# Performance work log

Hardware: AMD Instinct MI355X
Metric: run time of the kernel (lower is better)

Reference implementation:

```python
import jax, jax.numpy as jnp
import numpy as np

H = 512      # hidden_size
E = 256      # encoding_size
L = 64       # latent_dim
O = 2        # output_size
NH = 4       # num_heads
HD = H // NH # head dim
BS = 1024
S = 100      # encoded source length
T = 30       # decode steps


def setup_inputs() -> dict:
    key = jax.random.key(0)
    ks = jax.random.split(key, 26)
    def p(k, shape, s=0.05):
        return jax.random.normal(k, shape, dtype=jnp.float32) * s
    return {
        "encoded": jax.random.normal(ks[0], (BS, S, E), dtype=jnp.float32),
        "z": jax.random.normal(ks[1], (BS, T, L), dtype=jnp.float32),
        # MultiheadAttention params (separate q/k/v projections since kdim!=embed_dim)
        "q_w": p(ks[2], (H, H)), "k_w": p(ks[3], (H, E)), "v_w": p(ks[4], (H, E)),
        "q_b": p(ks[5], (H,)), "k_b": p(ks[6], (H,)), "v_b": p(ks[7], (H,)),
        "out_w": p(ks[8], (H, H)), "out_b": p(ks[9], (H,)),
        # fc_layer1: Linear(H+L, H)
        "fc1_w": p(ks[10], (H, H + L)), "fc1_b": p(ks[11], (H,)),
        # LSTMCell 1 and 2 (gate order i,f,g,o)
        "l1_wih": p(ks[12], (4 * H, H)), "l1_whh": p(ks[13], (4 * H, H)),
        "l1_bih": p(ks[14], (4 * H,)), "l1_bhh": p(ks[15], (4 * H,)),
        "l2_wih": p(ks[16], (4 * H, H)), "l2_whh": p(ks[17], (4 * H, H)),
        "l2_bih": p(ks[18], (4 * H,)), "l2_bhh": p(ks[19], (4 * H,)),
        # fc_layer2: H -> H/2 -> H/4 -> O
        "fc2a_w": p(ks[20], (H // 2, H)), "fc2a_b": p(ks[21], (H // 2,)),
        "fc2b_w": p(ks[22], (H // 4, H // 2)), "fc2b_b": p(ks[23], (H // 4,)),
        "fc2c_w": p(ks[24], (O, H // 4)), "fc2c_b": p(ks[25], (O,)),
    }


def _lrelu(x):
    return jnp.where(x >= 0, x, 0.2 * x)


def _lstm_cell(x, h, c, wih, whh, bih, bhh):
    g = x @ wih.T + bih + h @ whh.T + bhh
    i, f, gg, o = jnp.split(g, 4, axis=-1)
    c2 = jax.nn.sigmoid(f) * c + jax.nn.sigmoid(i) * jnp.tanh(gg)
    h2 = jax.nn.sigmoid(o) * jnp.tanh(c2)
    return h2, c2


def _forward(encoded, z, q_w, k_w, v_w, q_b, k_b, v_b, out_w, out_b,
             fc1_w, fc1_b, l1_wih, l1_whh, l1_bih, l1_bhh,
             l2_wih, l2_whh, l2_bih, l2_bhh,
             fc2a_w, fc2a_b, fc2b_w, fc2b_b, fc2c_w, fc2c_b):
    bs, s, _ = encoded.shape
    # K/V projections depend only on encoded -> compute once: [bs, NH, S, HD]
    k = (encoded @ k_w.T + k_b).reshape(bs, s, NH, HD).transpose(0, 2, 1, 3)
    v = (encoded @ v_w.T + v_b).reshape(bs, s, NH, HD).transpose(0, 2, 1, 3)
    scale = 1.0 / jnp.sqrt(jnp.float32(HD))

    def step(carry, zt):
        att_in, h1, c1, h2, c2 = carry  # all [bs, H]
        # single-query attention (query len 1); dropout inactive in eval
        q = ((att_in @ q_w.T + q_b) * scale).reshape(bs, NH, HD)
        attw = jax.nn.softmax(jnp.einsum('bnd,bnsd->bns', q, k), axis=-1)
        att = jnp.einsum('bns,bnsd->bnd', attw, v).reshape(bs, H)
        att = att @ out_w.T + out_b
        out = _lrelu(jnp.concatenate([att, zt], axis=-1) @ fc1_w.T + fc1_b)
        h1, c1 = _lstm_cell(out, h1, c1, l1_wih, l1_whh, l1_bih, l1_bhh)
        h2, c2 = _lstm_cell(h1, h2, c2, l2_wih, l2_whh, l2_bih, l2_bhh)
        y = _lrelu(h2 @ fc2a_w.T + fc2a_b)
        y = _lrelu(y @ fc2b_w.T + fc2b_b)
        y = jnp.tanh(y @ fc2c_w.T + fc2c_b)  # [bs, O]
        return (h2, h1, c1, h2, c2), y

    zer = jnp.zeros((bs, H), dtype=encoded.dtype)
    init = (zer, zer, zer, zer, zer)
    _, ys = jax.lax.scan(step, init, jnp.swapaxes(z, 0, 1))  # ys: [T, bs, O]
    return jnp.swapaxes(ys, 0, 1)  # [bs, T, O]


def reference(encoded, z, q_w, k_w, v_w, q_b, k_b, v_b, out_w, out_b,
              fc1_w, fc1_b, l1_wih, l1_whh, l1_bih, l1_bhh,
              l2_wih, l2_whh, l2_bih, l2_bhh,
              fc2a_w, fc2a_b, fc2b_w, fc2b_b, fc2c_w, fc2c_b):
    return _forward(encoded, z, q_w, k_w, v_w, q_b, k_b, v_b, out_w, out_b,
                    fc1_w, fc1_b, l1_wih, l1_whh, l1_bih, l1_bhh,
                    l2_wih, l2_whh, l2_bih, l2_bhh,
                    fc2a_w, fc2a_b, fc2b_w, fc2b_b, fc2c_w, fc2c_b)
```

## Files before the change

### kernel.cpp

```cpp
#include <hip/hip_runtime.h>


#define DEVI __device__ __forceinline__

typedef _Float16 f16x8 __attribute__((ext_vector_type(8)));
typedef _Float16 f16x4 __attribute__((ext_vector_type(4)));
typedef float    f32x4 __attribute__((ext_vector_type(4)));
typedef unsigned u32x4 __attribute__((ext_vector_type(4)));
typedef unsigned u32x2 __attribute__((ext_vector_type(2)));

#define BSZ 1024
#define SEQ 100
#define ENC 256
#define HID 512
#define LAT 64
#define TT  30

DEVI float lrelu(float v) { return v >= 0.f ? v : 0.2f * v; }
DEVI float sigm(float x)  { return 1.f / (1.f + __expf(-x)); }
DEVI float tanh_f(float x){ return 1.f - 2.f / (1.f + __expf(2.f * x)); }
DEVI unsigned umin2(unsigned a, unsigned b) { return a < b ? a : b; }

DEVI void wait_vm0() { asm volatile("s_waitcnt vmcnt(0)" ::: "memory"); }
DEVI u32x4 ld_sc_b128(const void* p) {
    u32x4 d;
    asm volatile("global_load_dwordx4 %0, %1, off sc0 sc1" : "=v"(d) : "v"(p) : "memory");
    return d;
}
DEVI void st_sc_b128(void* p, u32x4 v) {
    asm volatile("global_store_dwordx4 %0, %1, off sc0 sc1" :: "v"(p), "v"(v) : "memory");
}
DEVI void st_sc_b64(void* p, u32x2 v) {
    asm volatile("global_store_dwordx2 %0, %1, off sc0 sc1" :: "v"(p), "v"(v) : "memory");
}
DEVI void st_sc_b32(void* p, unsigned v) {
    asm volatile("global_store_dword %0, %1, off sc0 sc1" :: "v"(p), "v"(v) : "memory");
}

__global__ __launch_bounds__(256) void zero_ws(uint4* __restrict__ p) {
    uint4 z; z.x = z.y = z.z = z.w = 0u;
    p[(size_t)blockIdx.x * 256 + threadIdx.x] = z;
}

__global__ __launch_bounds__(256) void conv_enc(const float4* __restrict__ src,
                                                f16x4* __restrict__ dst) {
    size_t i = (size_t)blockIdx.x * 256 + threadIdx.x;
    float4 v = src[i];
    f16x4 h;
    h.x = (_Float16)v.x; h.y = (_Float16)v.y; h.z = (_Float16)v.z; h.w = (_Float16)v.w;
    dst[i] = h;
}

__global__ __launch_bounds__(256) void prep_qk(const float* __restrict__ k_w,
                                               const float* __restrict__ q_w,
                                               const float* __restrict__ q_b,
                                               _Float16* __restrict__ C_h,
                                               float* __restrict__ d_f,
                                               _Float16* __restrict__ d_h) {
    const int ne = blockIdx.x, n = ne >> 8, e = ne & 255, tid = threadIdx.x;
    const float scale = 0.08838834764831845f;
    float a0 = 0.f, a1 = 0.f;
    for (int dd = 0; dd < 128; ++dd) {
        float kv = k_w[(n * 128 + dd) * 256 + e];
        a0 += kv * q_w[(n * 128 + dd) * 512 + tid];
        a1 += kv * q_w[(n * 128 + dd) * 512 + 256 + tid];
    }
    C_h[(size_t)ne * 512 + tid]       = (_Float16)(scale * a0);
    C_h[(size_t)ne * 512 + 256 + tid] = (_Float16)(scale * a1);
    float pq = (tid < 128) ? k_w[(n * 128 + tid) * 256 + e] * q_b[n * 128 + tid] : 0.f;
    #pragma unroll
    for (int off = 32; off; off >>= 1) pq += __shfl_down(pq, off);
    __shared__ float red[4];
    if ((tid & 63) == 0) red[tid >> 6] = pq;
    __syncthreads();
    if (tid == 0) {
        float s = scale * (red[0] + red[1] + red[2] + red[3]);
        d_f[ne] = s; d_h[ne] = (_Float16)s;
    }
}

__global__ __launch_bounds__(256) void prep_A(const float* __restrict__ fc1_w,
                                              const float* __restrict__ out_w,
                                              float* __restrict__ A) {
    const int h = blockIdx.x, tid = threadIdx.x;
    float a0 = 0.f, a1 = 0.f;
    for (int m = 0; m < 512; ++m) {
        float fv = fc1_w[h * 576 + m];
        a0 += fv * out_w[m * 512 + tid];
        a1 += fv * out_w[m * 512 + 256 + tid];
    }
    A[(size_t)h * 512 + tid]       = a0;
    A[(size_t)h * 512 + 256 + tid] = a1;
}

__global__ __launch_bounds__(256) void prep_wfc1(const float* __restrict__ A,
                                                 const float* __restrict__ v_w,
                                                 const float* __restrict__ v_b,
                                                 const float* __restrict__ fc1_w,
                                                 const float* __restrict__ out_b,
                                                 const float* __restrict__ fc1_b,
                                                 _Float16* __restrict__ Wfc1,
                                                 float* __restrict__ biasf) {
    const int h = blockIdx.x, tid = threadIdx.x;
    #pragma unroll
    for (int g = 0; g < 4; ++g) {
        float acc = 0.f;
        for (int dd = 0; dd < 128; ++dd)
            acc += A[h * 512 + g * 128 + dd] * v_w[(g * 128 + dd) * 256 + tid];
        Wfc1[(size_t)h * 1088 + g * 256 + tid] = (_Float16)acc;
    }
    if (tid < 64)
        Wfc1[(size_t)h * 1088 + 1024 + tid] = (_Float16)fc1_w[h * 576 + 512 + tid];
    float ps = A[h * 512 + tid] * v_b[tid] + A[h * 512 + 256 + tid] * v_b[256 + tid]
             + fc1_w[h * 576 + tid] * out_b[tid] + fc1_w[h * 576 + 256 + tid] * out_b[256 + tid];
    #pragma unroll
    for (int off = 32; off; off >>= 1) ps += __shfl_down(ps, off);
    __shared__ float red[4];
    if ((tid & 63) == 0) red[tid >> 6] = ps;
    __syncthreads();
    if (tid == 0) biasf[h] = red[0] + red[1] + red[2] + red[3] + fc1_b[h];
}

__global__ __launch_bounds__(256) void prep_lstm(const float* __restrict__ wih,
                                                 const float* __restrict__ whh,
                                                 const float* __restrict__ bih,
                                                 const float* __restrict__ bhh,
                                                 _Float16* __restrict__ Wc,
                                                 float* __restrict__ bc) {
    int idx = blockIdx.x * 256 + threadIdx.x;
    int rp = idx >> 10, cc = idx & 1023;
    int h = rp >> 2, g = rp & 3;
    int rsrc = g * 512 + h;
    float v = (cc < 512) ? wih[(size_t)rsrc * 512 + cc] : whh[(size_t)rsrc * 512 + cc - 512];
    Wc[idx] = (_Float16)v;
    if (idx < 2048) {
        int h2 = idx >> 2, g2 = idx & 3;
        bc[idx] = bih[g2 * 512 + h2] + bhh[g2 * 512 + h2];
    }
}

__global__ __launch_bounds__(256) void prep_fc2c(const float* __restrict__ aw,
                                                 const float* __restrict__ bw,
                                                 const float* __restrict__ cw,
                                                 _Float16* __restrict__ a16,
                                                 _Float16* __restrict__ b16,
                                                 _Float16* __restrict__ c16) {
    int i = blockIdx.x * 256 + threadIdx.x;
    if (i < 131072) a16[i] = (_Float16)aw[i];
    else if (i < 163840) b16[i - 131072] = (_Float16)bw[i - 131072];
    else if (i < 164096) c16[i - 163840] = (_Float16)cw[i - 163840];
}

template <int NTHR, int BM, int BN, int BK, int WM, int WN, bool BYPX>
DEVI void gemm_core_db(char* smem_raw, const _Float16* __restrict__ X, int ldx,
                       const _Float16* __restrict__ W, int ldw, int K,
                       int bm0, int bn0, f32x4* acc) {
    constexpr int LDT = BK + 8;
    _Float16* Xs = (_Float16*)smem_raw;
    _Float16* Ws = Xs + BM * LDT;
    const int tid = threadIdx.x, wave = tid >> 6, lane = tid & 63;
    constexpr int WROWS = BM / WM;
    static_assert(WROWS * (BN / WN) == NTHR / 64, "wave grid mismatch");
    const int wm = wave % WROWS, wn = wave / WROWS;
    constexpr int MT = WM / 16, NT = WN / 16;
    const int q = lane >> 4, m15 = lane & 15;
    constexpr int CPR = BK / 8;
    constexpr int XCH = BM * CPR, WCH = BN * CPR;
    constexpr int XPT = (XCH + NTHR - 1) / NTHR;
    constexpr int WPT = (WCH + NTHR - 1) / NTHR;
    u32x4 xr[XPT], wr[WPT];
    auto ldregs = [&](int k0) {
        #pragma unroll
        for (int c = 0; c < XPT; ++c) {
            int cc = tid + c * NTHR;
            if ((XCH % NTHR) == 0 || cc < XCH) {
                int row = cc / CPR, col = (cc % CPR) * 8;
                const void* px = &X[(size_t)(bm0 + row) * ldx + k0 + col];
                if (BYPX) xr[c] = ld_sc_b128(px);
                else      xr[c] = *(const u32x4*)px;
            }
        }
        #pragma unroll
        for (int c = 0; c < WPT; ++c) {
            int cc = tid + c * NTHR;
            if ((WCH % NTHR) == 0 || cc < WCH) {
                int row = cc / CPR, col = (cc % CPR) * 8;
                wr[c] = *(const u32x4*)&W[(size_t)(bn0 + row) * ldw + k0 + col];
            }
        }
    };
    ldregs(0);
    for (int k0 = 0; k0 < K; k0 += BK) {
        if (BYPX) wait_vm0();
        #pragma unroll
        for (int c = 0; c < XPT; ++c) {
            int cc = tid + c * NTHR;
            if ((XCH % NTHR) == 0 || cc < XCH) {
                int row = cc / CPR, col = (cc % CPR) * 8;
                *(u32x4*)&Xs[row * LDT + col] = xr[c];
            }
        }
        #pragma unroll
        for (int c = 0; c < WPT; ++c) {
            int cc = tid + c * NTHR;
            if ((WCH % NTHR) == 0 || cc < WCH) {
                int row = cc / CPR, col = (cc % CPR) * 8;
                *(u32x4*)&Ws[row * LDT + col] = wr[c];
            }
        }
        __syncthreads();
        if (k0 + BK < K) ldregs(k0 + BK);
        #pragma unroll
        for (int kk = 0; kk < BK / 32; ++kk) {
            f16x8 af[MT], bf[NT];
            #pragma unroll
            for (int i = 0; i < MT; ++i)
                af[i] = *(const f16x8*)&Xs[(wm * WM + i * 16 + m15) * LDT + kk * 32 + q * 8];
            #pragma unroll
            for (int j = 0; j < NT; ++j)
                bf[j] = *(const f16x8*)&Ws[(wn * WN + j * 16 + m15) * LDT + kk * 32 + q * 8];
            #pragma unroll
            for (int i = 0; i < MT; ++i)
                #pragma unroll
                for (int j = 0; j < NT; ++j)
                    acc[i * NT + j] = __builtin_amdgcn_mfma_f32_16x16x32_f16(af[i], bf[j], acc[i * NT + j], 0, 0, 0);
        }
        __syncthreads();
    }
}

template <int NTHR, int BM, int BN, int WM, int WN, int ACT>
DEVI void epi_staged(char* smem_raw, const f32x4* acc, const float* __restrict__ bias,
                     _Float16* __restrict__ out, int ldo, int bm0, int bn0) {
    constexpr int LDS_ = BN + 4;
    float* accs = (float*)smem_raw;
    const int tid = threadIdx.x, wave = tid >> 6, lane = tid & 63;
    constexpr int WROWS = BM / WM;
    const int wm = wave % WROWS, wn = wave / WROWS;
    constexpr int MT = WM / 16, NT = WN / 16;
    const int q = lane >> 4, m15 = lane & 15;
    #pragma unroll
    for (int i = 0; i < MT; ++i) {
        #pragma unroll
        for (int j = 0; j < NT; ++j) {
            int cl = wn * WN + j * 16 + m15;
            float bv = bias[bn0 + cl];
            #pragma unroll
            for (int r = 0; r < 4; ++r) {
                int rl = wm * WM + i * 16 + q * 4 + r;
                float v = acc[i * NT + j][r] + bv;
                if (ACT == 1) v = lrelu(v);
                accs[rl * LDS_ + cl] = v;
            }
        }
    }
    __syncthreads();
    constexpr int CH = BN / 8, ITEMS = BM * CH;
    #pragma unroll
    for (int base = 0; base < ITEMS; base += NTHR) {
        int idx = base + tid;
        if ((ITEMS % NTHR) == 0 || idx < ITEMS) {
            int row = idx / CH, ch = idx % CH;
            const float* src = &accs[row * LDS_ + ch * 8];
            f16x8 o;
            #pragma unroll
            for (int k = 0; k < 8; ++k) o[k] = (_Float16)src[k];
            st_sc_b128(&out[(size_t)(bm0 + row) * ldo + bn0 + ch * 8],
                       __builtin_bit_cast(u32x4, o));
        }
    }
    __syncthreads();
}

DEVI void gbar(unsigned* bars, int grp, int sub, unsigned want) {
    wait_vm0();
    __syncthreads();
    if (threadIdx.x == 0) {
        st_sc_b32(&bars[grp * 16 + sub], want);
        unsigned spins = 0;
        for (;;) {
            u32x4 a = ld_sc_b128(&bars[grp * 16 + 0]);
            u32x4 b = ld_sc_b128(&bars[grp * 16 + 4]);
            u32x4 c = ld_sc_b128(&bars[grp * 16 + 8]);
            u32x4 d = ld_sc_b128(&bars[grp * 16 + 12]);
            wait_vm0();
            unsigned mn = umin2(umin2(umin2(a[0], a[1]), umin2(a[2], a[3])),
                          umin2(umin2(umin2(b[0], b[1]), umin2(b[2], b[3])),
                          umin2(umin2(umin2(c[0], c[1]), umin2(c[2], c[3])),
                                umin2(umin2(d[0], d[1]), umin2(d[2], d[3])))));
            if (mn >= want) break;
            __builtin_amdgcn_s_sleep(1);
            if (++spins > (1u << 17)) break;
        }
        asm volatile("" ::: "memory");
    }
    __syncthreads();
}

DEVI void attn_one(const _Float16* encs, const _Float16* gs, float* sc, float* wsm,
                   f32x4* part, const float* __restrict__ z,
                   _Float16* __restrict__ eb, int gi, int b, int t) {
    const int tid = threadIdx.x;
    {
        const int grpq = tid >> 4, l16 = tid & 15, n = grpq & 3, soff = grpq >> 2;
        const f16x8 g0 = *(const f16x8*)&gs[gi * 1024 + n * 256 + l16 * 8];
        const f16x8 g1 = *(const f16x8*)&gs[gi * 1024 + n * 256 + 128 + l16 * 8];
        for (int it = 0; it < 13; ++it) {
            int s = it * 8 + soff;
            if (s < SEQ) {
                const f16x8 e0 = *(const f16x8*)&encs[s * ENC + l16 * 8];
                const f16x8 e1 = *(const f16x8*)&encs[s * ENC + 128 + l16 * 8];
                float p = 0.f;
                #pragma unroll
                for (int j = 0; j < 8; ++j)
                    p += (float)e0[j] * (float)g0[j] + (float)e1[j] * (float)g1[j];
                p += __shfl_xor(p, 1); p += __shfl_xor(p, 2);
                p += __shfl_xor(p, 4); p += __shfl_xor(p, 8);
                if (l16 == 0) sc[n * 128 + s] = p;
            }
        }
    }
    __syncthreads();
    const int wv = tid >> 6, ln = tid & 63;
    if (wv < 4) {
        float v0 = sc[wv * 128 + ln];
        float v1 = (ln < SEQ - 64) ? sc[wv * 128 + 64 + ln] : -1e30f;
        float m = fmaxf(v0, v1);
        #pragma unroll
        for (int off = 32; off; off >>= 1) m = fmaxf(m, __shfl_xor(m, off));
        float e0 = __expf(v0 - m);
        float e1 = (ln < SEQ - 64) ? __expf(v1 - m) : 0.f;
        float ss = e0 + e1;
        #pragma unroll
        for (int off = 32; off; off >>= 1) ss += __shfl_xor(ss, off);
        float inv = 1.f / ss;
        wsm[wv * 128 + ln] = e0 * inv;
        if (ln < SEQ - 64) wsm[wv * 128 + 64 + ln] = e1 * inv;
    }
    __syncthreads();
    {
        const int n = wv & 3, half = wv >> 2;
        float a0 = 0.f, a1 = 0.f, a2 = 0.f, a3 = 0.f;
        const int sBeg = half * 50, sEnd = sBeg + 50;
        #pragma unroll 5
        for (int s = sBeg; s < sEnd; ++s) {
            f16x4 e4 = *(const f16x4*)&encs[s * ENC + ln * 4];
            float w = wsm[n * 128 + s];
            a0 += w * (float)e4.x; a1 += w * (float)e4.y;
            a2 += w * (float)e4.z; a3 += w * (float)e4.w;
        }
        f32x4 pv; pv[0] = a0; pv[1] = a1; pv[2] = a2; pv[3] = a3;
        part[wv * 64 + ln] = pv;
    }
    __syncthreads();
    if (tid < 128) {
        int n = tid >> 5, t8 = tid & 31;
        f32x4 a  = part[n * 64 + t8 * 2];
        f32x4 b2 = part[n * 64 + t8 * 2 + 1];
        f32x4 c  = part[(n + 4) * 64 + t8 * 2];
        f32x4 d  = part[(n + 4) * 64 + t8 * 2 + 1];
        f16x8 o;
        o[0] = (_Float16)(a[0] + c[0]); o[1] = (_Float16)(a[1] + c[1]);
        o[2] = (_Float16)(a[2] + c[2]); o[3] = (_Float16)(a[3] + c[3]);
        o[4] = (_Float16)(b2[0] + d[0]); o[5] = (_Float16)(b2[1] + d[1]);
        o[6] = (_Float16)(b2[2] + d[2]); o[7] = (_Float16)(b2[3] + d[3]);
        st_sc_b128(&eb[(size_t)b * 1088 + n * 256 + t8 * 8],
                   __builtin_bit_cast(u32x4, o));
    } else if (tid < 144) {
        int k = tid - 128;
        float4 zv = *(const float4*)&z[((size_t)b * TT + t) * 64 + k * 4];
        f16x4 zh;
        zh.x = (_Float16)zv.x; zh.y = (_Float16)zv.y;
        zh.z = (_Float16)zv.z; zh.w = (_Float16)zv.w;
        st_sc_b64(&eb[(size_t)b * 1088 + 1024 + k * 4],
                  __builtin_bit_cast(u32x2, zh));
    }
    __syncthreads();
}

DEVI void attn_phase(char* smem_all, u32x4 (&er)[3][7],
                     const _Float16* __restrict__ G, const float* __restrict__ z,
                     _Float16* __restrict__ eb, int b0, int t) {
    _Float16* encP  = (_Float16*)smem_all;
    char* scratch   = smem_all + 51200;
    _Float16* stage = (_Float16*)scratch;
    _Float16* gs    = (_Float16*)(scratch + 51200);
    float* sc       = (float*)(scratch + 59392);
    float* wsm      = (float*)(scratch + 61440);
    f32x4* part     = (f32x4*)(scratch + 63488);
    const int tid = threadIdx.x;
    {
        int row = tid >> 7, idx = tid & 127;
        u32x4 gv = ld_sc_b128(&G[(size_t)(b0 + row) * 1024 + idx * 8]);
        wait_vm0();
        *(u32x4*)&gs[row * 1024 + idx * 8] = gv;
    }
    __syncthreads();
    attn_one(encP, gs, sc, wsm, part, z, eb, 0, b0, t);
    #pragma unroll
    for (int i = 0; i < 3; ++i) {
        {
            u32x4* dst = (u32x4*)stage;
            #pragma unroll
            for (int k = 0; k < 6; ++k) dst[tid + k * 512] = er[i][k];
            if (tid < 128) dst[tid + 3072] = er[i][6];
        }
        __syncthreads();
        attn_one(stage, gs, sc, wsm, part, z, eb, i + 1, b0 + 1 + i, t);
    }
}

DEVI void lstm_phase(char* smem, const _Float16* __restrict__ X,
                     const _Float16* __restrict__ W, const float* __restrict__ bias,
                     float (&cr)[8], _Float16* __restrict__ hA, int ldA,
                     _Float16* __restrict__ hB, int ldB, int bm0, int bn0) {
    f32x4 acc[4] = {};
    gemm_core_db<512, 64, 128, 128, 32, 32, true>(smem, X, 1024, W, 1024, 1024, bm0, bn0, acc);
    float* accs = (float*)smem;
    const int tid = threadIdx.x, wave = tid >> 6, lane = tid & 63;
    const int wm = wave & 1, wn = wave >> 1, q = lane >> 4, m15 = lane & 15;
    #pragma unroll
    for (int i = 0; i < 2; ++i) {
        #pragma unroll
        for (int j = 0; j < 2; ++j) {
            int cl = wn * 32 + j * 16 + m15;
            float bv = bias[bn0 + cl];
            #pragma unroll
            for (int r = 0; r < 4; ++r) {
                int rl = wm * 32 + i * 16 + q * 4 + r;
                accs[rl * 132 + cl] = acc[i * 2 + j][r] + bv;
            }
        }
    }
    __syncthreads();
    if (tid < 256) {
        int bl = tid >> 2, ch = tid & 3;
        const float4* gp = (const float4*)&accs[bl * 132 + ch * 32];
        f16x8 hv;
        #pragma unroll
        for (int j = 0; j < 8; ++j) {
            float4 g4 = gp[j];
            float cn = sigm(g4.y) * cr[j] + sigm(g4.x) * tanh_f(g4.z);
            cr[j] = cn;
            hv[j] = (_Float16)(sigm(g4.w) * tanh_f(cn));
        }
        int h0 = (bn0 >> 2) + ch * 8, gb = bm0 + bl;
        u32x4 hb = __builtin_bit_cast(u32x4, hv);
        st_sc_b128(&hA[(size_t)gb * ldA + h0], hb);
        st_sc_b128(&hB[(size_t)gb * ldB + h0], hb);
    }
    __syncthreads();
}

DEVI void fc2_512(char* smem, const _Float16* __restrict__ h2n,
                  const _Float16* __restrict__ Wa, const float* __restrict__ ab,
                  const _Float16* __restrict__ Wb, const float* __restrict__ bb,
                  const _Float16* __restrict__ Wc, const float* __restrict__ cb,
                  float* __restrict__ out, int b0, int t) {
    _Float16* h2s = (_Float16*)smem;
    _Float16* y1s = h2s + 16 * 520;
    _Float16* y2s = y1s + 16 * 264;
    const int tid = threadIdx.x, wave = tid >> 6, lane = tid & 63;
    const int q = lane >> 4, m15 = lane & 15;
    u32x4 hv[2];
    #pragma unroll
    for (int c = 0; c < 2; ++c) {
        int cc = tid + c * 512, row = cc >> 6, col = (cc & 63) * 8;
        hv[c] = ld_sc_b128(&h2n[(size_t)(b0 + row) * 512 + col]);
    }
    wait_vm0();
    #pragma unroll
    for (int c = 0; c < 2; ++c) {
        int cc = tid + c * 512, row = cc >> 6, col = (cc & 63) * 8;
        *(u32x4*)&h2s[row * 520 + col] = hv[c];
    }
    __syncthreads();
    {
        f32x4 acc[2] = {};
        #pragma unroll 4
        for (int kk = 0; kk < 16; ++kk) {
            f16x8 af = *(const f16x8*)&h2s[m15 * 520 + kk * 32 + q * 8];
            #pragma unroll
            for (int j = 0; j < 2; ++j) {
                int n = wave * 32 + j * 16 + m15;
                f16x8 bf = *(const f16x8*)&Wa[(size_t)n * 512 + kk * 32 + q * 8];
                acc[j] = __builtin_amdgcn_mfma_f32_16x16x32_f16(af, bf, acc[j], 0, 0, 0);
            }
        }
        #pragma unroll
        for (int j = 0; j < 2; ++j) {
            int col = wave * 32 + j * 16 + m15;
            float bv = ab[col];
            #pragma unroll
            for (int r = 0; r < 4; ++r)
                y1s[(q * 4 + r) * 264 + col] = (_Float16)lrelu(acc[j][r] + bv);
        }
    }
    __syncthreads();
    {
        f32x4 acc[1] = {};
        #pragma unroll
        for (int kk = 0; kk < 8; ++kk) {
            f16x8 af = *(const f16x8*)&y1s[m15 * 264 + kk * 32 + q * 8];
            int n = wave * 16 + m15;
            f16x8 bf = *(const f16x8*)&Wb[(size_t)n * 256 + kk * 32 + q * 8];
            acc[0] = __builtin_amdgcn_mfma_f32_16x16x32_f16(af, bf, acc[0], 0, 0, 0);
        }
        int col = wave * 16 + m15;
        float bv = bb[col];
        #pragma unroll
        for (int r = 0; r < 4; ++r)
            y2s[(q * 4 + r) * 136 + col] = (_Float16)lrelu(acc[0][r] + bv);
    }
    __syncthreads();
    if (tid < 32) {
        int r = tid >> 1, o = tid & 1;
        float acc = cb[o];
        #pragma unroll 8
        for (int k = 0; k < 128; ++k)
            acc += (float)Wc[o * 128 + k] * (float)y2s[r * 136 + k];
        out[((size_t)(b0 + r) * TT + t) * 2 + o] = tanhf(acc);
    }
}

struct DecP {
    const _Float16* encH;
    const float* z;
    _Float16* eb;
    const _Float16* Wfc1;  const float* biasf;
    const _Float16* L1W;   const float* L1b;
    const _Float16* L2W;   const float* L2b;
    const _Float16* C_h;   const float* d_f;  const _Float16* d_h;
    const _Float16* fa;    const float* fab;
    const _Float16* fb;    const float* fbb;
    const _Float16* fcw;   const float* fcb;
    _Float16* xh1[2];  _Float16* xh2[2];  _Float16* h2n;  _Float16* G;
    float* out;
    unsigned* bars;
};

__global__ __launch_bounds__(512, 1) void decoder(DecP p) {
    __shared__ __align__(16) char smem[122880];
    char* scratch = smem + 51200;
    const int blk = blockIdx.x, tid = threadIdx.x;
    const int grp = blk >> 4, sub = blk & 15;
    const int b0a = blk * 4;
    const int bm0 = grp * 64;
    float c1r[8] = {}, c2r[8] = {};
    u32x4 er[3][7];
    unsigned want = 0;
    {
        const u32x4* s0 = (const u32x4*)(p.encH + (size_t)b0a * (SEQ * ENC));
        u32x4* encP = (u32x4*)smem;
        #pragma unroll
        for (int k = 0; k < 6; ++k) encP[tid + k * 512] = s0[tid + k * 512];
        if (tid < 128) encP[tid + 3072] = s0[tid + 3072];
        #pragma unroll
        for (int i = 0; i < 3; ++i) {
            const u32x4* si = (const u32x4*)(p.encH + (size_t)(b0a + 1 + i) * (SEQ * ENC));
            #pragma unroll
            for (int k = 0; k < 6; ++k) er[i][k] = si[tid + k * 512];
            if (tid < 128) er[i][6] = si[tid + 3072];
        }
    }
    if (tid < 128) {
        u32x4 v = *(const u32x4*)&p.d_h[tid * 8];
        #pragma unroll
        for (int i = 0; i < 4; ++i)
            st_sc_b128(&p.G[(size_t)(b0a + i) * 1024 + tid * 8], v);
    }
    wait_vm0();
    __syncthreads();
    for (int t = 0; t < TT; ++t) {
        const int pt = t & 1;
        attn_phase(smem, er, p.G, p.z, p.eb, b0a, t);
        gbar(p.bars, grp, sub, ++want);
        {
            f32x4 acc[1] = {};
            gemm_core_db<512, 64, 32, 64, 16, 16, true>(scratch, p.eb, 1088, p.Wfc1, 1088, 1088,
                                                        bm0, sub * 32, acc);
            epi_staged<512, 64, 32, 16, 16, 1>(scratch, acc, p.biasf, p.xh1[pt], 1024, bm0, sub * 32);
        }
        gbar(p.bars, grp, sub, ++want);
        lstm_phase(scratch, p.xh1[pt], p.L1W, p.L1b, c1r,
                   p.xh2[pt], 1024, p.xh1[pt ^ 1] + 512, 1024, bm0, sub * 128);
        gbar(p.bars, grp, sub, ++want);
        lstm_phase(scratch, p.xh2[pt], p.L2W, p.L2b, c2r,
                   p.h2n, 512, p.xh2[pt ^ 1] + 512, 1024, bm0, sub * 128);
        gbar(p.bars, grp, sub, ++want);
        if (t < TT - 1) {
            f32x4 acc[2] = {};
            gemm_core_db<512, 64, 64, 128, 16, 32, true>(scratch, p.h2n, 512, p.C_h, 512, 512,
                                                         bm0, sub * 64, acc);
            epi_staged<512, 64, 64, 16, 32, 0>(scratch, acc, p.d_f, p.G, 1024, bm0, sub * 64);
        }
        if (sub < 4)
            fc2_512(scratch, p.h2n, p.fa, p.fab, p.fb, p.fbb, p.fcw, p.fcb,
                    p.out, bm0 + sub * 16, t);
        if (t < TT - 1) gbar(p.bars, grp, sub, ++want);
    }
}

extern "C" void kernel_launch(void* const* d_in, const int* in_sizes, int n_in,
                              void* d_out, int out_size, void* d_ws, size_t ws_size,
                              hipStream_t stream) {
    const float* encoded = (const float*)d_in[0];
    const float* z       = (const float*)d_in[1];
    const float* q_w     = (const float*)d_in[2];
    const float* k_w     = (const float*)d_in[3];
    const float* v_w     = (const float*)d_in[4];
    const float* q_b     = (const float*)d_in[5];
    const float* v_b     = (const float*)d_in[7];
    const float* out_w   = (const float*)d_in[8];
    const float* out_b   = (const float*)d_in[9];
    const float* fc1_w   = (const float*)d_in[10];
    const float* fc1_b   = (const float*)d_in[11];
    const float* l1_wih  = (const float*)d_in[12];
    const float* l1_whh  = (const float*)d_in[13];
    const float* l1_bih  = (const float*)d_in[14];
    const float* l1_bhh  = (const float*)d_in[15];
    const float* l2_wih  = (const float*)d_in[16];
    const float* l2_whh  = (const float*)d_in[17];
    const float* l2_bih  = (const float*)d_in[18];
    const float* l2_bhh  = (const float*)d_in[19];
    const float* fc2a_w  = (const float*)d_in[20];
    const float* fc2a_b  = (const float*)d_in[21];
    const float* fc2b_w  = (const float*)d_in[22];
    const float* fc2b_b  = (const float*)d_in[23];
    const float* fc2c_w  = (const float*)d_in[24];
    const float* fc2c_b  = (const float*)d_in[25];
    float* out = (float*)d_out;

    char* p = (char*)d_ws;
    auto take = [&](size_t bytes) { char* r = p; p += (bytes + 255) & ~(size_t)255; return r; };
    _Float16* encH  = (_Float16*)take(52428800);
    _Float16* C_h   = (_Float16*)take(1048576);
    _Float16* Wfc1  = (_Float16*)take(1114112);
    _Float16* L1W   = (_Float16*)take(4194304);
    _Float16* L2W   = (_Float16*)take(4194304);
    _Float16* fc2a16= (_Float16*)take(262144);
    _Float16* fc2b16= (_Float16*)take(65536);
    _Float16* fc2c16= (_Float16*)take(512);
    _Float16* eb    = (_Float16*)take(2228224);
    _Float16* h2n   = (_Float16*)take(1048576);
    char* zreg = p;
    _Float16* xh1a = (_Float16*)take(2097152);
    _Float16* xh1b = (_Float16*)take(2097152);
    _Float16* xh2a = (_Float16*)take(2097152);
    _Float16* xh2b = (_Float16*)take(2097152);
    unsigned* bars = (unsigned*)take(4096);
    _Float16* G   = (_Float16*)take(2097152);
    float* A      = (float*)take(1048576);
    float* d_f    = (float*)take(4096);
    _Float16* d_h = (_Float16*)take(2048);
    float* biasf  = (float*)take(2048);
    float* L1b    = (float*)take(8192);
    float* L2b    = (float*)take(8192);
    (void)in_sizes; (void)n_in; (void)out_size; (void)ws_size;

    zero_ws<<<2049, 256, 0, stream>>>((uint4*)zreg);
    conv_enc<<<25600, 256, 0, stream>>>((const float4*)encoded, (f16x4*)encH);
    prep_qk<<<1024, 256, 0, stream>>>(k_w, q_w, q_b, C_h, d_f, d_h);
    prep_A<<<512, 256, 0, stream>>>(fc1_w, out_w, A);
    prep_wfc1<<<512, 256, 0, stream>>>(A, v_w, v_b, fc1_w, out_b, fc1_b, Wfc1, biasf);
    prep_lstm<<<8192, 256, 0, stream>>>(l1_wih, l1_whh, l1_bih, l1_bhh, L1W, L1b);
    prep_lstm<<<8192, 256, 0, stream>>>(l2_wih, l2_whh, l2_bih, l2_bhh, L2W, L2b);
    prep_fc2c<<<641, 256, 0, stream>>>(fc2a_w, fc2b_w, fc2c_w, fc2a16, fc2b16, fc2c16);

    DecP dp;
    dp.encH = encH; dp.z = z; dp.eb = eb;
    dp.Wfc1 = Wfc1; dp.biasf = biasf;
    dp.L1W = L1W; dp.L1b = L1b; dp.L2W = L2W; dp.L2b = L2b;
    dp.C_h = C_h; dp.d_f = d_f; dp.d_h = d_h;
    dp.fa = fc2a16; dp.fab = fc2a_b; dp.fb = fc2b16; dp.fbb = fc2b_b;
    dp.fcw = fc2c16; dp.fcb = fc2c_b;
    dp.xh1[0] = xh1a; dp.xh1[1] = xh1b;
    dp.xh2[0] = xh2a; dp.xh2[1] = xh2b;
    dp.h2n = h2n; dp.G = G;
    dp.out = out; dp.bars = bars;
    void* params[] = { &dp };
    if (hipLaunchCooperativeKernel((const void*)decoder, dim3(256), dim3(512),
                                   params, 0, stream) != hipSuccess) {
        decoder<<<256, 512, 0, stream>>>(dp);
    }
}
```

Before: 3.133 ms.

## Keep two encoder rows in LDS and stream the rest from global per step

Instead of holding three encoder rows in registers (er[3][7]) and one in LDS, the kernel now keeps two encoder batch rows resident in an enlarged LDS buffer. It reloads the other two from global memory each step, prefetching each into registers while the previous attention body runs. The attention weighted-sum now uses only four waves over the full sequence, with no partial-sum reduction pass and its extra barrier. This frees a large block of registers and trims the synchronisation, at the cost of re-reading two encoder rows per step from L2/HBM and using more LDS.

```diff
diff --git a/kernel.cpp b/kernel.cpp
--- a/kernel.cpp
+++ b/kernel.cpp
@@ -297,14 +297,14 @@
     __syncthreads();
 }
 
-DEVI void attn_one(const _Float16* encs, const _Float16* gs, float* sc, float* wsm,
-                   f32x4* part, const float* __restrict__ z,
-                   _Float16* __restrict__ eb, int gi, int b, int t) {
+DEVI void attn_body(const _Float16* encs, const _Float16* gs, float* sc, float* wsm,
+                    const float* __restrict__ z, _Float16* __restrict__ eb,
+                    int b, int t) {
     const int tid = threadIdx.x;
     {
         const int grpq = tid >> 4, l16 = tid & 15, n = grpq & 3, soff = grpq >> 2;
-        const f16x8 g0 = *(const f16x8*)&gs[gi * 1024 + n * 256 + l16 * 8];
-        const f16x8 g1 = *(const f16x8*)&gs[gi * 1024 + n * 256 + 128 + l16 * 8];
+        const f16x8 g0 = *(const f16x8*)&gs[n * 256 + l16 * 8];
+        const f16x8 g1 = *(const f16x8*)&gs[n * 256 + 128 + l16 * 8];
         for (int it = 0; it < 13; ++it) {
             int s = it * 8 + soff;
             if (s < SEQ) {
@@ -338,76 +338,72 @@
         if (ln < SEQ - 64) wsm[wv * 128 + 64 + ln] = e1 * inv;
     }
     __syncthreads();
-    {
-        const int n = wv & 3, half = wv >> 2;
+    if (wv < 4) {
         float a0 = 0.f, a1 = 0.f, a2 = 0.f, a3 = 0.f;
-        const int sBeg = half * 50, sEnd = sBeg + 50;
         #pragma unroll 5
-        for (int s = sBeg; s < sEnd; ++s) {
+        for (int s = 0; s < SEQ; ++s) {
             f16x4 e4 = *(const f16x4*)&encs[s * ENC + ln * 4];
-            float w = wsm[n * 128 + s];
+            float w = wsm[wv * 128 + s];
             a0 += w * (float)e4.x; a1 += w * (float)e4.y;
             a2 += w * (float)e4.z; a3 += w * (float)e4.w;
         }
-        f32x4 pv; pv[0] = a0; pv[1] = a1; pv[2] = a2; pv[3] = a3;
-        part[wv * 64 + ln] = pv;
-    }
-    __syncthreads();
-    if (tid < 128) {
-        int n = tid >> 5, t8 = tid & 31;
-        f32x4 a  = part[n * 64 + t8 * 2];
-        f32x4 b2 = part[n * 64 + t8 * 2 + 1];
-        f32x4 c  = part[(n + 4) * 64 + t8 * 2];
-        f32x4 d  = part[(n + 4) * 64 + t8 * 2 + 1];
-        f16x8 o;
-        o[0] = (_Float16)(a[0] + c[0]); o[1] = (_Float16)(a[1] + c[1]);
-        o[2] = (_Float16)(a[2] + c[2]); o[3] = (_Float16)(a[3] + c[3]);
-        o[4] = (_Float16)(b2[0] + d[0]); o[5] = (_Float16)(b2[1] + d[1]);
-        o[6] = (_Float16)(b2[2] + d[2]); o[7] = (_Float16)(b2[3] + d[3]);
-        st_sc_b128(&eb[(size_t)b * 1088 + n * 256 + t8 * 8],
-                   __builtin_bit_cast(u32x4, o));
-    } else if (tid < 144) {
-        int k = tid - 128;
-        float4 zv = *(const float4*)&z[((size_t)b * TT + t) * 64 + k * 4];
+        f16x4 o;
+        o.x = (_Float16)a0; o.y = (_Float16)a1; o.z = (_Float16)a2; o.w = (_Float16)a3;
+        st_sc_b64(&eb[(size_t)b * 1088 + wv * 256 + ln * 4],
+                  __builtin_bit_cast(u32x2, o));
+    } else if (wv == 4 && ln < 16) {
+        float4 zv = *(const float4*)&z[((size_t)b * TT + t) * 64 + ln * 4];
         f16x4 zh;
         zh.x = (_Float16)zv.x; zh.y = (_Float16)zv.y;
         zh.z = (_Float16)zv.z; zh.w = (_Float16)zv.w;
-        st_sc_b64(&eb[(size_t)b * 1088 + 1024 + k * 4],
+        st_sc_b64(&eb[(size_t)b * 1088 + 1024 + ln * 4],
                   __builtin_bit_cast(u32x2, zh));
     }
     __syncthreads();
 }
 
-DEVI void attn_phase(char* smem_all, u32x4 (&er)[3][7],
-                     const _Float16* __restrict__ G, const float* __restrict__ z,
+DEVI void attn_phase(char* smem, const _Float16* __restrict__ G,
+                     const _Float16* __restrict__ encH, const float* __restrict__ z,
                      _Float16* __restrict__ eb, int b0, int t) {
-    _Float16* encP  = (_Float16*)smem_all;
-    char* scratch   = smem_all + 51200;
-    _Float16* stage = (_Float16*)scratch;
-    _Float16* gs    = (_Float16*)(scratch + 51200);
-    float* sc       = (float*)(scratch + 59392);
-    float* wsm      = (float*)(scratch + 61440);
-    f32x4* part     = (f32x4*)(scratch + 63488);
+    _Float16* encP0 = (_Float16*)smem;
+    _Float16* encP1 = (_Float16*)(smem + 51200);
+    float* sc       = (float*)(smem + 102400);
+    float* wsm      = (float*)(smem + 104448);
+    _Float16* gs    = (_Float16*)(smem + 106496);
+    _Float16* stage = (_Float16*)(smem + 108544);
     const int tid = threadIdx.x;
-    {
-        int row = tid >> 7, idx = tid & 127;
-        u32x4 gv = ld_sc_b128(&G[(size_t)(b0 + row) * 1024 + idx * 8]);
-        wait_vm0();
-        *(u32x4*)&gs[row * 1024 + idx * 8] = gv;
-    }
-    __syncthreads();
-    attn_one(encP, gs, sc, wsm, part, z, eb, 0, b0, t);
-    #pragma unroll
-    for (int i = 0; i < 3; ++i) {
-        {
-            u32x4* dst = (u32x4*)stage;
-            #pragma unroll
-            for (int k = 0; k < 6; ++k) dst[tid + k * 512] = er[i][k];
-            if (tid < 128) dst[tid + 3072] = er[i][6];
-        }
-        __syncthreads();
-        attn_one(stage, gs, sc, wsm, part, z, eb, i + 1, b0 + 1 + i, t);
-    }
+    const int grow = tid >> 7, gidx = tid & 127;
+    u32x4 gv = ld_sc_b128(&G[(size_t)(b0 + grow) * 1024 + gidx * 8]);
+    u32x4 r[7];
+    auto ldenc = [&](int b) {
+        const u32x4* src = (const u32x4*)(encH + (size_t)b * (SEQ * ENC));
+        #pragma unroll
+        for (int i = 0; i < 6; ++i) r[i] = src[tid + i * 512];
+        if (tid < 128) r[6] = src[tid + 3072];
+    };
+    auto stage_r = [&]() {
+        u32x4* dst = (u32x4*)stage;
+        #pragma unroll
+        for (int k = 0; k < 6; ++k) dst[tid + k * 512] = r[k];
+        if (tid < 128) dst[tid + 3072] = r[6];
+    };
+    wait_vm0();
+    if (grow == 0) *(u32x4*)&gs[gidx * 8] = gv;
+    __syncthreads();
+    ldenc(b0 + 2);
+    attn_body(encP0, gs, sc, wsm, z, eb, b0, t);
+    if (grow == 1) *(u32x4*)&gs[gidx * 8] = gv;
+    __syncthreads();
+    attn_body(encP1, gs, sc, wsm, z, eb, b0 + 1, t);
+    stage_r();
+    if (grow == 2) *(u32x4*)&gs[gidx * 8] = gv;
+    __syncthreads();
+    ldenc(b0 + 3);
+    attn_body(stage, gs, sc, wsm, z, eb, b0 + 2, t);
+    stage_r();
+    if (grow == 3) *(u32x4*)&gs[gidx * 8] = gv;
+    __syncthreads();
+    attn_body(stage, gs, sc, wsm, z, eb, b0 + 3, t);
 }
 
 DEVI void lstm_phase(char* smem, const _Float16* __restrict__ X,
@@ -540,27 +536,27 @@
 };
 
 __global__ __launch_bounds__(512, 1) void decoder(DecP p) {
-    __shared__ __align__(16) char smem[122880];
-    char* scratch = smem + 51200;
+    __shared__ __align__(16) char smem[160768];
+    char* scratch = smem + 108544;
     const int blk = blockIdx.x, tid = threadIdx.x;
     const int grp = blk >> 4, sub = blk & 15;
     const int b0a = blk * 4;
     const int bm0 = grp * 64;
     float c1r[8] = {}, c2r[8] = {};
-    u32x4 er[3][7];
     unsigned want = 0;
     {
         const u32x4* s0 = (const u32x4*)(p.encH + (size_t)b0a * (SEQ * ENC));
-        u32x4* encP = (u32x4*)smem;
-        #pragma unroll
-        for (int k = 0; k < 6; ++k) encP[tid + k * 512] = s0[tid + k * 512];
-        if (tid < 128) encP[tid + 3072] = s0[tid + 3072];
-        #pragma unroll
-        for (int i = 0; i < 3; ++i) {
-            const u32x4* si = (const u32x4*)(p.encH + (size_t)(b0a + 1 + i) * (SEQ * ENC));
-            #pragma unroll
-            for (int k = 0; k < 6; ++k) er[i][k] = si[tid + k * 512];
-            if (tid < 128) er[i][6] = si[tid + 3072];
+        const u32x4* s1 = (const u32x4*)(p.encH + (size_t)(b0a + 1) * (SEQ * ENC));
+        u32x4* d0 = (u32x4*)smem;
+        u32x4* d1 = (u32x4*)(smem + 51200);
+        #pragma unroll
+        for (int k = 0; k < 6; ++k) {
+            d0[tid + k * 512] = s0[tid + k * 512];
+            d1[tid + k * 512] = s1[tid + k * 512];
+        }
+        if (tid < 128) {
+            d0[tid + 3072] = s0[tid + 3072];
+            d1[tid + 3072] = s1[tid + 3072];
         }
     }
     if (tid < 128) {
@@ -573,7 +569,7 @@
     __syncthreads();
     for (int t = 0; t < TT; ++t) {
         const int pt = t & 1;
-        attn_phase(smem, er, p.G, p.z, p.eb, b0a, t);
+        attn_phase(smem, p.G, p.encH, p.z, p.eb, b0a, t);
         gbar(p.bars, grp, sub, ++want);
         {
             f32x4 acc[1] = {};
```

Measured after the change: 3.250 ms. +3.7%, slower.
